# Kernel optimization log

Measured on AMD Instinct MI355X. Metric: run time of the kernel, lower is better.

Reference implementation:

```python
import jax, jax.numpy as jnp
import numpy as np

B, D, H, DEPTH = 1024, 1024, 1024, 4


def setup_inputs() -> dict:
    key = jax.random.key(0)
    k_x, k_w, k_ws, k_bs = jax.random.split(key, 4)
    x = jax.random.normal(k_x, (B, D), dtype=jnp.float32)
    W_enc = jax.random.normal(k_w, (D, H), dtype=jnp.float32) * 0.02
    b_enc = jnp.zeros((H,), dtype=jnp.float32)
    # per-layer CrossNet weights, matching keras random_normal init (stddev=0.05)
    ws = jax.random.normal(k_ws, (DEPTH, H, 1), dtype=jnp.float32) * 0.05
    bs = jax.random.normal(k_bs, (DEPTH, H, 1), dtype=jnp.float32) * 0.05
    return {"x": x, "W_enc": W_enc, "b_enc": b_enc, "ws": ws, "bs": bs}


def reference(x, W_enc, b_enc, ws, bs):
    # encoder Dense
    h = jnp.matmul(x, W_enc) + b_enc  # (B, H)
    x0 = h
    x_l = h
    depth = ws.shape[0]
    for l in range(depth):
        # original: (x0[:, :, None] * x_l[:, None, :]) @ w + b, squeezed.
        # outer[b,i,j] @ w  == x0[b,i] * sum_j x_l[b,j] * w[j]
        s = jnp.matmul(x_l, ws[l])            # (B, 1)
        residual = x0 * s + bs[l][:, 0]       # (B, H)
        x_l = residual + x_l
    return x_l
```

## Files before the change

### kernel.cpp

```cpp
#include <hip/hip_runtime.h>
#include <hip/hip_bf16.h>


#define DEPTH 4

typedef _Float16 half4_t __attribute__((ext_vector_type(4)));
typedef _Float16 half8_t __attribute__((ext_vector_type(8)));
typedef float floatx4_t __attribute__((ext_vector_type(4)));

typedef const __attribute__((address_space(1))) unsigned int* gas_ptr;
typedef __attribute__((address_space(3))) unsigned int* las_ptr;

__device__ __forceinline__ void async_copy16(const void* g, void* l) {
    __builtin_amdgcn_global_load_lds((gas_ptr)g, (las_ptr)l, 16, 0, 0);
}

__device__ __forceinline__ half4_t cvt4(float4 f) {
    half4_t o;
    o.x = (_Float16)f.x; o.y = (_Float16)f.y;
    o.z = (_Float16)f.z; o.w = (_Float16)f.w;
    return o;
}
__device__ __forceinline__ float dot4(float4 a, float4 b) {
    return a.x * b.x + a.y * b.y + a.z * b.z + a.w * b.w;
}

__global__ __launch_bounds__(256) void prep_kernel(
        const float* __restrict__ x, const float* __restrict__ W,
        const float* __restrict__ b_enc, const float* __restrict__ ws,
        const float* __restrict__ bs, _Float16* __restrict__ xh,
        _Float16* __restrict__ Wt, float* __restrict__ v,
        float* __restrict__ eg, float* __restrict__ Bsum) {
    const int b = blockIdx.x;
    const int t = threadIdx.x;
    if (b < 256) {
        __shared__ float S[64][65];
        const int k0 = (b >> 4) << 6;
        const int n0 = (b & 15) << 6;
#pragma unroll
        for (int i = 0; i < 4; ++i) {
            int idx = (i << 8) + t;
            int r = idx >> 4;
            int c4 = idx & 15;
            float4 vv = *(const float4*)(W + (size_t)(k0 + r) * 1024 + n0 + (c4 << 2));
            S[r][(c4 << 2) + 0] = vv.x;
            S[r][(c4 << 2) + 1] = vv.y;
            S[r][(c4 << 2) + 2] = vv.z;
            S[r][(c4 << 2) + 3] = vv.w;
        }
        __syncthreads();
#pragma unroll
        for (int i = 0; i < 4; ++i) {
            int idx = (i << 8) + t;
            int n = idx >> 4;
            int c4 = idx & 15;
            int k = c4 << 2;
            half4_t o;
            o.x = (_Float16)S[k + 0][n];
            o.y = (_Float16)S[k + 1][n];
            o.z = (_Float16)S[k + 2][n];
            o.w = (_Float16)S[k + 3][n];
            *(half4_t*)(Wt + (size_t)(n0 + n) * 1024 + k0 + k) = o;
        }
    } else if (b < 512) {
        const int base = (b - 256) << 12;
#pragma unroll
        for (int i = 0; i < 4; ++i) {
            int off = base + (((i << 8) + t) << 2);
            *(half4_t*)(xh + off) = cvt4(*(const float4*)(x + off));
        }
    } else if (b < 640) {
        const int row = ((b - 512) << 3) + (t >> 5);
        const int l32 = t & 31;
        const float* Wr = W + (size_t)row * 1024 + (l32 << 2);
        float vp[4] = {0.f, 0.f, 0.f, 0.f};
#pragma unroll
        for (int i = 0; i < 8; ++i) {
            float4 wr = *(const float4*)(Wr + (i << 7));
#pragma unroll
            for (int l = 0; l < 4; ++l) {
                float4 wl = *(const float4*)(ws + l * 1024 + (l32 << 2) + (i << 7));
                vp[l] += dot4(wr, wl);
            }
        }
#pragma unroll
        for (int l = 0; l < 4; ++l)
#pragma unroll
            for (int off = 16; off > 0; off >>= 1)
                vp[l] += __shfl_down(vp[l], off, 32);
        if (l32 == 0) {
#pragma unroll
            for (int l = 0; l < 4; ++l) v[l * 1024 + row] = vp[l];
        }
    } else {
        __shared__ float egred[4][7];
        const int c = t << 2;
        float4 w0 = *(const float4*)(ws + c);
        float4 w1 = *(const float4*)(ws + 1024 + c);
        float4 w2 = *(const float4*)(ws + 2048 + c);
        float4 w3 = *(const float4*)(ws + 3072 + c);
        float4 q0 = *(const float4*)(bs + c);
        float4 q1 = *(const float4*)(bs + 1024 + c);
        float4 q2 = *(const float4*)(bs + 2048 + c);
        float4 q3 = *(const float4*)(bs + 3072 + c);
        float4 ben = *(const float4*)(b_enc + c);
        float4 B2, B3, Bs;
        B2.x = q0.x + q1.x; B2.y = q0.y + q1.y; B2.z = q0.z + q1.z; B2.w = q0.w + q1.w;
        B3.x = B2.x + q2.x; B3.y = B2.y + q2.y; B3.z = B2.z + q2.z; B3.w = B2.w + q2.w;
        Bs.x = B3.x + q3.x; Bs.y = B3.y + q3.y; Bs.z = B3.z + q3.z; Bs.w = B3.w + q3.w;
        *(float4*)(Bsum + c) = Bs;
        float vals[7];
        vals[0] = dot4(ben, w0); vals[1] = dot4(ben, w1);
        vals[2] = dot4(ben, w2); vals[3] = dot4(ben, w3);
        vals[4] = dot4(q0, w1);  vals[5] = dot4(B2, w2); vals[6] = dot4(B3, w3);
#pragma unroll
        for (int i = 0; i < 7; ++i)
#pragma unroll
            for (int off = 32; off > 0; off >>= 1)
                vals[i] += __shfl_down(vals[i], off, 64);
        if ((t & 63) == 0)
#pragma unroll
            for (int i = 0; i < 7; ++i) egred[t >> 6][i] = vals[i];
        __syncthreads();
        if (t == 0) {
#pragma unroll
            for (int i = 0; i < 4; ++i)
                eg[i] = egred[0][i] + egred[1][i] + egred[2][i] + egred[3][i];
            eg[4] = 0.f;
#pragma unroll
            for (int i = 4; i < 7; ++i)
                eg[i + 1] = egred[0][i] + egred[1][i] + egred[2][i] + egred[3][i];
        }
    }
}

__global__ __launch_bounds__(256) void gemm_kernel(
        const _Float16* __restrict__ xh, const _Float16* __restrict__ Wt,
        const float* __restrict__ b_enc, const float* __restrict__ v,
        const float* __restrict__ eg, const float* __restrict__ Bsum,
        float* __restrict__ out) {
    __shared__ _Float16 G[2][6144];
    __shared__ float4 dred[32];
    __shared__ float a4s[32];
    const int t    = threadIdx.x;
    const int lane = t & 63;
    const int w    = t >> 6;
    const int m0 = (blockIdx.x >> 4) << 5;
    const int n0 = (blockIdx.x & 15) << 6;
    const int wm = (w >> 1) << 4;
    const int wn = (w & 1) << 5;

    const int sr = t >> 3;
    const int sc = ((t & 7) ^ (sr & 7)) << 3;
    const _Float16* aSrc  = xh + (size_t)(m0 + sr) * 1024 + sc;
    const _Float16* bSrc0 = Wt + (size_t)(n0 + sr) * 1024 + sc;
    const _Float16* bSrc1 = Wt + (size_t)(n0 + sr + 32) * 1024 + sc;

    async_copy16(aSrc,  &G[0][(w << 9)]);
    async_copy16(bSrc0, &G[0][2048 + (w << 9)]);
    async_copy16(bSrc1, &G[0][4096 + (w << 9)]);

    {
        const int kc = lane;
        float d[8][4];
#pragma unroll
        for (int j = 0; j < 8; ++j)
#pragma unroll
            for (int l = 0; l < 4; ++l) d[j][l] = 0.f;
#pragma unroll
        for (int i = 0; i < 2; ++i) {
            const int k = (kc << 4) + (i << 3);
            float4 vv[4][2];
#pragma unroll
            for (int l = 0; l < 4; ++l) {
                vv[l][0] = *(const float4*)(v + l * 1024 + k);
                vv[l][1] = *(const float4*)(v + l * 1024 + k + 4);
            }
#pragma unroll
            for (int j = 0; j < 8; ++j) {
                half8_t a = *(const half8_t*)(xh + (size_t)(m0 + (w << 3) + j) * 1024 + k);
                float af[8];
#pragma unroll
                for (int e2 = 0; e2 < 8; ++e2) af[e2] = (float)a[e2];
#pragma unroll
                for (int l = 0; l < 4; ++l)
                    d[j][l] += af[0] * vv[l][0].x + af[1] * vv[l][0].y
                             + af[2] * vv[l][0].z + af[3] * vv[l][0].w
                             + af[4] * vv[l][1].x + af[5] * vv[l][1].y
                             + af[6] * vv[l][1].z + af[7] * vv[l][1].w;
            }
        }
#pragma unroll
        for (int j = 0; j < 8; ++j)
#pragma unroll
            for (int l = 0; l < 4; ++l)
#pragma unroll
                for (int off = 32; off > 0; off >>= 1)
                    d[j][l] += __shfl_down(d[j][l], off, 64);
        if (lane == 0)
#pragma unroll
            for (int j = 0; j < 8; ++j) {
                float4 dd = {d[j][0], d[j][1], d[j][2], d[j][3]};
                dred[(w << 3) + j] = dd;
            }
    }
    __syncthreads();
    if (t < 32) {
        float4 D = dred[t];
        float4 e = *(const float4*)(eg);
        float4 g = *(const float4*)(eg + 4);
        float d0 = D.x + e.x, d1 = D.y + e.y, d2 = D.z + e.z, d3 = D.w + e.w;
        float a = 1.f;
        a += a * d0 + g.x;
        a += a * d1 + g.y;
        a += a * d2 + g.z;
        a += a * d3 + g.w;
        a4s[t] = a;
    }

    const int cq = lane & 15;
    const int q  = lane >> 4;
    const int ra  = wm + cq;
    const int rb0 = wn + cq;
    const int rb1 = wn + 16 + cq;
    floatx4_t acc0 = {0.f, 0.f, 0.f, 0.f};
    floatx4_t acc1 = {0.f, 0.f, 0.f, 0.f};

    for (int it = 0; it < 16; ++it) {
        __syncthreads();
        if (it + 1 < 16) {
            const int kk = (it + 1) << 6;
            _Float16* Gb = G[(it + 1) & 1];
            async_copy16(aSrc + kk,  Gb + (w << 9));
            async_copy16(bSrc0 + kk, Gb + 2048 + (w << 9));
            async_copy16(bSrc1 + kk, Gb + 4096 + (w << 9));
        }
        const _Float16* Gb = G[it & 1];
#pragma unroll
        for (int kc2 = 0; kc2 < 2; ++kc2) {
            const int lc = (kc2 << 2) + q;
            half8_t af  = *(const half8_t*)(Gb + ra * 64 + ((lc ^ (ra & 7)) << 3));
            half8_t bf0 = *(const half8_t*)(Gb + 2048 + rb0 * 64 + ((lc ^ (rb0 & 7)) << 3));
            half8_t bf1 = *(const half8_t*)(Gb + 2048 + rb1 * 64 + ((lc ^ (rb1 & 7)) << 3));
            acc0 = __builtin_amdgcn_mfma_f32_16x16x32_f16(af, bf0, acc0, 0, 0, 0);
            acc1 = __builtin_amdgcn_mfma_f32_16x16x32_f16(af, bf1, acc1, 0, 0, 0);
        }
    }

    const int col0 = n0 + wn + cq;
    const int col1 = col0 + 16;
    const int row0 = m0 + wm + (q << 2);
    float4 a4f = *(const float4*)(&a4s[wm + (q << 2)]);
    float a4a[4] = {a4f.x, a4f.y, a4f.z, a4f.w};
    float be0 = b_enc[col0], be1 = b_enc[col1];
    float Bs0 = Bsum[col0],  Bs1 = Bsum[col1];
#pragma unroll
    for (int r = 0; r < 4; ++r) {
        out[(size_t)(row0 + r) * 1024 + col0] = a4a[r] * (acc0[r] + be0) + Bs0;
        out[(size_t)(row0 + r) * 1024 + col1] = a4a[r] * (acc1[r] + be1) + Bs1;
    }
}

extern "C" void kernel_launch(void* const* d_in, const int* in_sizes, int n_in,
                              void* d_out, int out_size, void* d_ws, size_t ws_size,
                              hipStream_t stream) {
    const float* x     = (const float*)d_in[0];
    const float* W_enc = (const float*)d_in[1];
    const float* b_enc = (const float*)d_in[2];
    const float* ws    = (const float*)d_in[3];
    const float* bs    = (const float*)d_in[4];
    float* out = (float*)d_out;

    _Float16* xh = (_Float16*)d_ws;
    _Float16* Wt = xh + (1 << 20);
    float*    v    = (float*)((char*)d_ws + (4u << 20));
    float*    eg   = v + 4096;
    float*    Bsum = eg + 8;

    prep_kernel<<<641, 256, 0, stream>>>(x, W_enc, b_enc, ws, bs,
                                         xh, Wt, v, eg, Bsum);
    gemm_kernel<<<512, 256, 0, stream>>>(xh, Wt, b_enc, v, eg, Bsum, out);
}
```

Measured before the change: 89.41 us.

## Fold per-row dot products with v into the main MFMA loop

The gemm kernel used to compute the per-row projections x·v for the four layers with a separate scalar FP32 prologue that read xh from global memory and did shuffle reductions. Now v is stored as fp16, staged in shared memory, and fed to a third MFMA per k-step that reuses the A fragment already in LDS. The row scale factor is then built from the MFMA result in the epilogue. This removes the prologue's global loads and reductions but adds MFMA work, a new LDS buffer, and fp16 rounding of v, which may cost accuracy.

```diff
diff --git a/kernel.cpp b/kernel.cpp
--- a/kernel.cpp
+++ b/kernel.cpp
@@ -29,7 +29,7 @@
         const float* __restrict__ x, const float* __restrict__ W,
         const float* __restrict__ b_enc, const float* __restrict__ ws,
         const float* __restrict__ bs, _Float16* __restrict__ xh,
-        _Float16* __restrict__ Wt, float* __restrict__ v,
+        _Float16* __restrict__ Wt, _Float16* __restrict__ vh,
         float* __restrict__ eg, float* __restrict__ Bsum) {
     const int b = blockIdx.x;
     const int t = threadIdx.x;
@@ -90,7 +90,7 @@
                 vp[l] += __shfl_down(vp[l], off, 32);
         if (l32 == 0) {
 #pragma unroll
-            for (int l = 0; l < 4; ++l) v[l * 1024 + row] = vp[l];
+            for (int l = 0; l < 4; ++l) vh[(l << 10) + row] = (_Float16)vp[l];
         }
     } else {
         __shared__ float egred[4][7];
@@ -136,12 +136,12 @@
 
 __global__ __launch_bounds__(256) void gemm_kernel(
         const _Float16* __restrict__ xh, const _Float16* __restrict__ Wt,
-        const float* __restrict__ b_enc, const float* __restrict__ v,
+        const float* __restrict__ b_enc, const _Float16* __restrict__ vh,
         const float* __restrict__ eg, const float* __restrict__ Bsum,
         float* __restrict__ out) {
     __shared__ _Float16 G[2][6144];
-    __shared__ float4 dred[32];
-    __shared__ float a4s[32];
+    __shared__ _Float16 vhs[4][1032];
+    __shared__ float dS[32][4];
     const int t    = threadIdx.x;
     const int lane = t & 63;
     const int w    = t >> 6;
@@ -159,63 +159,13 @@
     async_copy16(aSrc,  &G[0][(w << 9)]);
     async_copy16(bSrc0, &G[0][2048 + (w << 9)]);
     async_copy16(bSrc1, &G[0][4096 + (w << 9)]);
-
     {
-        const int kc = lane;
-        float d[8][4];
-#pragma unroll
-        for (int j = 0; j < 8; ++j)
-#pragma unroll
-            for (int l = 0; l < 4; ++l) d[j][l] = 0.f;
-#pragma unroll
-        for (int i = 0; i < 2; ++i) {
-            const int k = (kc << 4) + (i << 3);
-            float4 vv[4][2];
-#pragma unroll
-            for (int l = 0; l < 4; ++l) {
-                vv[l][0] = *(const float4*)(v + l * 1024 + k);
-                vv[l][1] = *(const float4*)(v + l * 1024 + k + 4);
-            }
-#pragma unroll
-            for (int j = 0; j < 8; ++j) {
-                half8_t a = *(const half8_t*)(xh + (size_t)(m0 + (w << 3) + j) * 1024 + k);
-                float af[8];
-#pragma unroll
-                for (int e2 = 0; e2 < 8; ++e2) af[e2] = (float)a[e2];
-#pragma unroll
-                for (int l = 0; l < 4; ++l)
-                    d[j][l] += af[0] * vv[l][0].x + af[1] * vv[l][0].y
-                             + af[2] * vv[l][0].z + af[3] * vv[l][0].w
-                             + af[4] * vv[l][1].x + af[5] * vv[l][1].y
-                             + af[6] * vv[l][1].z + af[7] * vv[l][1].w;
-            }
-        }
-#pragma unroll
-        for (int j = 0; j < 8; ++j)
-#pragma unroll
-            for (int l = 0; l < 4; ++l)
-#pragma unroll
-                for (int off = 32; off > 0; off >>= 1)
-                    d[j][l] += __shfl_down(d[j][l], off, 64);
-        if (lane == 0)
-#pragma unroll
-            for (int j = 0; j < 8; ++j) {
-                float4 dd = {d[j][0], d[j][1], d[j][2], d[j][3]};
-                dred[(w << 3) + j] = dd;
-            }
-    }
-    __syncthreads();
-    if (t < 32) {
-        float4 D = dred[t];
-        float4 e = *(const float4*)(eg);
-        float4 g = *(const float4*)(eg + 4);
-        float d0 = D.x + e.x, d1 = D.y + e.y, d2 = D.z + e.z, d3 = D.w + e.w;
-        float a = 1.f;
-        a += a * d0 + g.x;
-        a += a * d1 + g.y;
-        a += a * d2 + g.z;
-        a += a * d3 + g.w;
-        a4s[t] = a;
+        const int r  = t >> 6;
+        const int ln = t & 63;
+        *(half8_t*)(&vhs[r][ln << 3]) =
+            *(const half8_t*)(vh + (r << 10) + (ln << 3));
+        *(half8_t*)(&vhs[r][(ln << 3) + 512]) =
+            *(const half8_t*)(vh + (r << 10) + (ln << 3) + 512);
     }
 
     const int cq = lane & 15;
@@ -223,8 +173,11 @@
     const int ra  = wm + cq;
     const int rb0 = wn + cq;
     const int rb1 = wn + 16 + cq;
+    const _Float16* vrow = &vhs[cq & 3][q << 3];
+
     floatx4_t acc0 = {0.f, 0.f, 0.f, 0.f};
     floatx4_t acc1 = {0.f, 0.f, 0.f, 0.f};
+    floatx4_t dacc = {0.f, 0.f, 0.f, 0.f};
 
     for (int it = 0; it < 16; ++it) {
         __syncthreads();
@@ -242,22 +195,36 @@
             half8_t af  = *(const half8_t*)(Gb + ra * 64 + ((lc ^ (ra & 7)) << 3));
             half8_t bf0 = *(const half8_t*)(Gb + 2048 + rb0 * 64 + ((lc ^ (rb0 & 7)) << 3));
             half8_t bf1 = *(const half8_t*)(Gb + 2048 + rb1 * 64 + ((lc ^ (rb1 & 7)) << 3));
+            half8_t vf  = *(const half8_t*)(vrow + (it << 6) + (kc2 << 5));
             acc0 = __builtin_amdgcn_mfma_f32_16x16x32_f16(af, bf0, acc0, 0, 0, 0);
             acc1 = __builtin_amdgcn_mfma_f32_16x16x32_f16(af, bf1, acc1, 0, 0, 0);
-        }
-    }
-
+            dacc = __builtin_amdgcn_mfma_f32_16x16x32_f16(af, vf, dacc, 0, 0, 0);
+        }
+    }
+
+    if (((w & 1) == 0) && cq < 4) {
+#pragma unroll
+        for (int r = 0; r < 4; ++r) dS[wm + (q << 2) + r][cq] = dacc[r];
+    }
+    __syncthreads();
+
+    const float4 e  = *(const float4*)(eg);
+    const float4 g4 = *(const float4*)(eg + 4);
     const int col0 = n0 + wn + cq;
     const int col1 = col0 + 16;
     const int row0 = m0 + wm + (q << 2);
-    float4 a4f = *(const float4*)(&a4s[wm + (q << 2)]);
-    float a4a[4] = {a4f.x, a4f.y, a4f.z, a4f.w};
-    float be0 = b_enc[col0], be1 = b_enc[col1];
-    float Bs0 = Bsum[col0],  Bs1 = Bsum[col1];
+    const float be0 = b_enc[col0], be1 = b_enc[col1];
+    const float Bs0 = Bsum[col0],  Bs1 = Bsum[col1];
 #pragma unroll
     for (int r = 0; r < 4; ++r) {
-        out[(size_t)(row0 + r) * 1024 + col0] = a4a[r] * (acc0[r] + be0) + Bs0;
-        out[(size_t)(row0 + r) * 1024 + col1] = a4a[r] * (acc1[r] + be1) + Bs1;
+        float4 dv = *(const float4*)(&dS[wm + (q << 2) + r][0]);
+        float a = 1.f;
+        a += a * (dv.x + e.x) + g4.x;
+        a += a * (dv.y + e.y) + g4.y;
+        a += a * (dv.z + e.z) + g4.z;
+        a += a * (dv.w + e.w) + g4.w;
+        out[(size_t)(row0 + r) * 1024 + col0] = a * (acc0[r] + be0) + Bs0;
+        out[(size_t)(row0 + r) * 1024 + col1] = a * (acc1[r] + be1) + Bs1;
     }
 }
 
@@ -273,11 +240,11 @@
 
     _Float16* xh = (_Float16*)d_ws;
     _Float16* Wt = xh + (1 << 20);
-    float*    v    = (float*)((char*)d_ws + (4u << 20));
-    float*    eg   = v + 4096;
+    _Float16* vh = Wt + (1 << 20);
+    float*    eg   = (float*)((char*)d_ws + (4u << 20) + 8192);
     float*    Bsum = eg + 8;
 
     prep_kernel<<<641, 256, 0, stream>>>(x, W_enc, b_enc, ws, bs,
-                                         xh, Wt, v, eg, Bsum);
-    gemm_kernel<<<512, 256, 0, stream>>>(xh, Wt, b_enc, v, eg, Bsum, out);
-}
+                                         xh, Wt, vh, eg, Bsum);
+    gemm_kernel<<<512, 256, 0, stream>>>(xh, Wt, b_enc, vh, eg, Bsum, out);
+}
```

Measured after the change: 84.51 us. 1.06x faster.
